# Kernel optimization log

Hardware: AMD Instinct MI355X
Metric: run time of the kernel (lower is better)

The kernel has to match this reference:

```python
import jax, jax.numpy as jnp
import numpy as np

B, S, D, H = 2, 2048, 768, 12
DH = D // H  # 64


def setup_inputs() -> dict:
    key = jax.random.key(0)
    ks = jax.random.split(key, 6)
    sd = 1.0 / np.sqrt(D)
    x = jax.random.normal(ks[0], (B, S, 3 * D), dtype=jnp.float32)
    # causal additive mask: 1.0 where attention is disallowed (future positions)
    mask = jnp.triu(jnp.ones((S, S), dtype=jnp.float32), k=1)[None, None, :, :]
    return {
        "x": x,
        "mask": mask,
        "wq": jax.random.normal(ks[1], (D, D), dtype=jnp.float32) * sd,
        "bq": jnp.zeros((D,), dtype=jnp.float32),
        "wk": jax.random.normal(ks[2], (D, D), dtype=jnp.float32) * sd,
        "bk": jnp.zeros((D,), dtype=jnp.float32),
        "wv": jax.random.normal(ks[3], (D, D), dtype=jnp.float32) * sd,
        "bv": jnp.zeros((D,), dtype=jnp.float32),
        "wc": jax.random.normal(ks[4], (D, D), dtype=jnp.float32) * sd,
        "bc": jnp.zeros((D,), dtype=jnp.float32),
    }


def _split_heads(t):
    # [B, S, D] -> [B, H, S, DH]
    return t.reshape(B, S, H, DH).transpose(0, 2, 1, 3)


def reference(x, mask, wq, bq, wk, bk, wv, bv, wc, bc):
    xq, xk, xv = jnp.split(x, 3, axis=-1)
    q = _split_heads(xq @ wq + bq)
    k = _split_heads(xk @ wk + bk)
    v = _split_heads(xv @ wv + bv)
    scores = jnp.einsum("bhqd,bhkd->bhqk", q, k) / jnp.sqrt(jnp.float32(DH))
    scores = scores + mask * (-1e9)
    attn = jax.nn.softmax(scores, axis=-1)
    out = jnp.einsum("bhqk,bhkd->bhqd", attn, v)
    out = out.transpose(0, 2, 1, 3).reshape(B, S, D)  # merge heads
    return out @ wc + bc
```

## Files before the change

### kernel.cpp

```cpp
#include <hip/hip_runtime.h>
#include <math.h>

#define S_LEN   2048
#define D_MODEL 768
#define NH      12
#define DH      64
#define BATCH   2

typedef __attribute__((ext_vector_type(4)))  float f32x4;
typedef __attribute__((ext_vector_type(16))) float f32x16;
typedef __attribute__((ext_vector_type(8)))  short bf16x8;
typedef __attribute__((ext_vector_type(4)))  short short4v;
typedef __attribute__((ext_vector_type(2)))  unsigned u32x2;

__device__ __forceinline__ short f2bf(float f) {
    union { float f; unsigned u; } v; v.f = f;
    unsigned r = (v.u + 0x7FFFu + ((v.u >> 16) & 1u)) >> 16;
    return (short)r;
}
__device__ __forceinline__ float bf2f(short s) {
    union { unsigned u; float f; } v; v.u = ((unsigned)(unsigned short)s) << 16;
    return v.f;
}
__device__ __forceinline__ unsigned cvt_pk_bf16(float lo, float hi) {
    unsigned r;
    asm("v_cvt_pk_bf16_f32 %0, %1, %2" : "=v"(r) : "v"(lo), "v"(hi));
    return r;
}
__device__ __forceinline__ void perm32swap(unsigned &a, unsigned &b) {
    asm("v_permlane32_swap_b32 %0, %1" : "+v"(a), "+v"(b));
}

#define GLOAD_LDS16(gp, lp)                                                     \
    __builtin_amdgcn_global_load_lds(                                           \
        (const __attribute__((address_space(1))) void*)(gp),                    \
        (__attribute__((address_space(3))) void*)(lp), 16, 0, 0)

__global__ __launch_bounds__(256) void convert_xw_kernel(
    const float* __restrict__ x, short* __restrict__ xb,
    const float* __restrict__ wq, const float* __restrict__ wk,
    const float* __restrict__ wv, const float* __restrict__ wc,
    short* __restrict__ wt)
{
    const int bid = blockIdx.x;
    const int t = threadIdx.x;
    if (bid < 4608) {
        const size_t i = ((size_t)bid * 256 + t) * 8;
        const f32x4 a = *(const f32x4*)(x + i);
        const f32x4 b = *(const f32x4*)(x + i + 4);
        bf16x8 r;
        r[0] = f2bf(a[0]); r[1] = f2bf(a[1]); r[2] = f2bf(a[2]); r[3] = f2bf(a[3]);
        r[4] = f2bf(b[0]); r[5] = f2bf(b[1]); r[6] = f2bf(b[2]); r[7] = f2bf(b[3]);
        *(bf16x8*)(xb + i) = r;
        return;
    }
    __shared__ float Ld[64][65];
    const int rem = bid - 4608;
    const int z  = rem / 144;
    const int yy = (rem % 144) / 12;
    const int xx = rem % 12;
    const float* W = (z == 0) ? wq : (z == 1) ? wk : (z == 2) ? wv : wc;
    short* dst = wt + (size_t)z * D_MODEL * D_MODEL;
    const int r0 = yy * 64;
    const int c0 = xx * 64;

#pragma unroll
    for (int i = 0; i < 4; ++i) {
        const int r = (t >> 4) + 16 * i;
        const int c = (t & 15) * 4;
        const float4 a = *(const float4*)(W + (size_t)(r0 + r) * D_MODEL + c0 + c);
        Ld[r][c + 0] = a.x; Ld[r][c + 1] = a.y; Ld[r][c + 2] = a.z; Ld[r][c + 3] = a.w;
    }
    __syncthreads();
#pragma unroll
    for (int i = 0; i < 4; ++i) {
        const int n = (t >> 4) + 16 * i;
        const int kq = (t & 15) * 4;
        short4v s4;
        s4[0] = f2bf(Ld[kq + 0][n]); s4[1] = f2bf(Ld[kq + 1][n]);
        s4[2] = f2bf(Ld[kq + 2][n]); s4[3] = f2bf(Ld[kq + 3][n]);
        *(short4v*)(dst + (size_t)(c0 + n) * D_MODEL + r0 + kq) = s4;
    }
}

__device__ __forceinline__ void gemm_bt_body(
    const short* __restrict__ A, int lda,
    const short* __restrict__ Bt,
    const float* __restrict__ bias,
    void* __restrict__ C, int ldc, int out_mode)
{
    __shared__ __align__(16) char ldsA[16384];
    __shared__ __align__(16) char ldsB[16384];

    const int t = threadIdx.x, lane = t & 63, w = t >> 6;
    const int l15 = lane & 15, l4 = lane >> 4;
    const int wr = w >> 1, wc = w & 1;
    const int row0 = blockIdx.y * 128, col0 = blockIdx.x * 128;

    const int srow = lane >> 3;
    const int sblk = (lane & 7) ^ srow;

    f32x4 acc[4][4];
#pragma unroll
    for (int i = 0; i < 4; ++i)
#pragma unroll
        for (int j = 0; j < 4; ++j) acc[i][j] = (f32x4){0.f, 0.f, 0.f, 0.f};

    for (int kt = 0; kt < 12; ++kt) {
        __syncthreads();
#pragma unroll
        for (int i = 0; i < 4; ++i) {
            const int row = i * 32 + w * 8 + srow;
            GLOAD_LDS16(A  + (size_t)(row0 + row) * lda + kt * 64 + sblk * 8,
                        ldsA + i * 4096 + w * 1024);
            GLOAD_LDS16(Bt + (size_t)(col0 + row) * D_MODEL + kt * 64 + sblk * 8,
                        ldsB + i * 4096 + w * 1024);
        }
        __syncthreads();

        bf16x8 af[4][2], bfr[4][2];
#pragma unroll
        for (int rb = 0; rb < 4; ++rb) {
            const int r = wr * 64 + rb * 16 + l15;
#pragma unroll
            for (int c = 0; c < 2; ++c)
                af[rb][c] = *(const bf16x8*)(ldsA + r * 128 + (((c * 4 + l4) ^ (r & 7)) << 4));
        }
#pragma unroll
        for (int cb = 0; cb < 4; ++cb) {
            const int r = wc * 64 + cb * 16 + l15;
#pragma unroll
            for (int c = 0; c < 2; ++c)
                bfr[cb][c] = *(const bf16x8*)(ldsB + r * 128 + (((c * 4 + l4) ^ (r & 7)) << 4));
        }
        __builtin_amdgcn_s_setprio(1);
#pragma unroll
        for (int rb = 0; rb < 4; ++rb)
#pragma unroll
            for (int cb = 0; cb < 4; ++cb) {
                acc[rb][cb] = __builtin_amdgcn_mfma_f32_16x16x32_bf16(
                    af[rb][0], bfr[cb][0], acc[rb][cb], 0, 0, 0);
                acc[rb][cb] = __builtin_amdgcn_mfma_f32_16x16x32_bf16(
                    af[rb][1], bfr[cb][1], acc[rb][cb], 0, 0, 0);
            }
        __builtin_amdgcn_s_setprio(0);
    }

#pragma unroll
    for (int cb = 0; cb < 4; ++cb) {
        const int col = col0 + wc * 64 + cb * 16 + l15;
        const float bv = bias[col];
        if (out_mode == 2) {
            const int h  = col >> 6, dh = col & 63;
#pragma unroll
            for (int rb = 0; rb < 4; ++rb) {
                const int row = row0 + wr * 64 + rb * 16 + 4 * l4;
                const int b   = row >> 11, s0 = row & 2047;
                short4v s4;
                s4[0] = f2bf(acc[rb][cb][0] + bv);
                s4[1] = f2bf(acc[rb][cb][1] + bv);
                s4[2] = f2bf(acc[rb][cb][2] + bv);
                s4[3] = f2bf(acc[rb][cb][3] + bv);
                *(short4v*)((short*)C + ((size_t)((b * 12 + h) * 64 + dh)) * S_LEN + s0) = s4;
            }
        } else {
#pragma unroll
            for (int rb = 0; rb < 4; ++rb)
#pragma unroll
                for (int r = 0; r < 4; ++r) {
                    const int row = row0 + wr * 64 + rb * 16 + 4 * l4 + r;
                    const float val = acc[rb][cb][r] + bv;
                    if (out_mode == 1) ((short*)C)[(size_t)row * ldc + col] = f2bf(val);
                    else               ((float*)C)[(size_t)row * ldc + col] = val;
                }
        }
    }
}

__global__ __launch_bounds__(256) void qkv_gemm_kernel(
    const short* __restrict__ xb, const short* __restrict__ wt,
    const float* __restrict__ bq, const float* __restrict__ bk,
    const float* __restrict__ bv, short* __restrict__ qkv)
{
    const int which = blockIdx.z;
    const float* bias = (which == 0) ? bq : (which == 1) ? bk : bv;
    gemm_bt_body(xb + which * D_MODEL, 3 * D_MODEL,
                 wt + (size_t)which * D_MODEL * D_MODEL, bias,
                 qkv + (size_t)which * BATCH * S_LEN * D_MODEL, D_MODEL,
                 (which == 2) ? 2 : 1);
}

__global__ __launch_bounds__(256) void proj_gemm_kernel(
    const short* __restrict__ att, const short* __restrict__ wct,
    const float* __restrict__ bc, float* __restrict__ out)
{
    gemm_bt_body(att, D_MODEL, wct, bc, out, D_MODEL, 0);
}

__global__ __launch_bounds__(512, 4) void attn_mfma_kernel(
    const short* __restrict__ q, const short* __restrict__ k,
    const short* __restrict__ vt, short* __restrict__ o)
{
    __shared__ __align__(16) char bufK[2][2][8192];
    __shared__ __align__(16) char bufV[2][2][8192];
    __shared__ float mlx[2][128];

    const int t    = threadIdx.x;
    const int lane = t & 63;
    const int w    = t >> 6;
    const int g    = w >> 2;
    const int w4   = w & 3;
    const int l31  = lane & 31;
    const int hi   = lane >> 5;
    const int r7   = l31 & 7;

    const int h  = blockIdx.y;
    const int b  = blockIdx.z;
    const int bh = h + 12 * b;
    const int qt = (bh >= 16) ? (15 - (int)blockIdx.x) : (int)blockIdx.x;
    const int nt = qt + 1;

    const size_t base   = (size_t)b * (S_LEN * D_MODEL) + h * DH;
    const size_t vtbase = (size_t)bh * DH * S_LEN;
    const int q0 = qt * 128 + w4 * 32;

    bf16x8 qf[4];
    {
        const short* qp = q + base + (size_t)(q0 + l31) * D_MODEL + 8 * hi;
#pragma unroll
        for (int dc = 0; dc < 4; ++dc) {
            bf16x8 r = *(const bf16x8*)(qp + 16 * dc);
#pragma unroll
            for (int j = 0; j < 8; ++j) r[j] = f2bf(bf2f(r[j]) * 0.125f);
            qf[dc] = r;
        }
    }

    f32x16 oT[2];
    oT[0] = (f32x16)(0.f); oT[1] = (f32x16)(0.f);
    float mrun = -1e30f, lrun = 0.f;

    const int srow = lane >> 3;
    const int sblk = (lane & 7) ^ srow;

    {
        const int tk0 = g * nt;
#pragma unroll
        for (int i = 0; i < 2; ++i) {
            const int row = i * 32 + w4 * 8 + srow;
            GLOAD_LDS16(k  + base   + (size_t)(tk0 * 64 + row) * D_MODEL + sblk * 8,
                        bufK[g][0] + i * 4096 + w4 * 1024);
            GLOAD_LDS16(vt + vtbase + (size_t)row * S_LEN + tk0 * 64 + sblk * 8,
                        bufV[g][0] + i * 4096 + w4 * 1024);
        }
        __syncthreads();
    }

    for (int i = 0; i < nt; ++i) {
        const int cur = i & 1, nxt = cur ^ 1;
        const bool have_next = (i + 1 < nt);
        const int tk = g * nt + i;

        if (have_next) {
            const int tkn = tk + 1;
#pragma unroll
            for (int j = 0; j < 2; ++j) {
                const int row = j * 32 + w4 * 8 + srow;
                GLOAD_LDS16(k  + base   + (size_t)(tkn * 64 + row) * D_MODEL + sblk * 8,
                            bufK[g][nxt] + (size_t)(j * 4096 + w4 * 1024));
                GLOAD_LDS16(vt + vtbase + (size_t)row * S_LEN + tkn * 64 + sblk * 8,
                            bufV[g][nxt] + (size_t)(j * 4096 + w4 * 1024));
            }
        }

        if (tk * 64 <= q0 + 31) {
            f32x16 cS[2];
            __builtin_amdgcn_s_setprio(1);
#pragma unroll
            for (int s = 0; s < 2; ++s) {
                f32x16 acc = (f32x16)(0.f);
#pragma unroll
                for (int dc = 0; dc < 4; ++dc) {
                    const int row = 32 * s + l31;
                    const bf16x8 kf = *(const bf16x8*)(
                        bufK[g][cur] + row * 128 + (((unsigned)(32 * dc + 16 * hi)) ^ ((unsigned)r7 << 4)));
                    acc = __builtin_amdgcn_mfma_f32_32x32x16_bf16(kf, qf[dc], acc, 0, 0, 0);
                }
                cS[s] = acc;
            }
            __builtin_amdgcn_s_setprio(0);

            if (tk * 64 + 63 > q0) {
                const int qg = q0 + l31;
#pragma unroll
                for (int s = 0; s < 2; ++s)
#pragma unroll
                    for (int rg = 0; rg < 16; ++rg) {
                        const int key = tk * 64 + 32 * s + (rg & 3) + 8 * (rg >> 2) + 4 * hi;
                        if (key > qg) cS[s][rg] = -1e30f;
                    }
            }

            float pmax = -1e30f;
#pragma unroll
            for (int s = 0; s < 2; ++s)
#pragma unroll
                for (int rg = 0; rg < 16; ++rg) pmax = fmaxf(pmax, cS[s][rg]);
            pmax = fmaxf(pmax, __shfl_xor(pmax, 32));

            if (!__all(pmax - mrun <= 8.0f)) {
                const float mnew = fmaxf(mrun, pmax);
                const float corr = __expf(mrun - mnew);
                lrun *= corr;
#pragma unroll
                for (int d0 = 0; d0 < 2; ++d0)
#pragma unroll
                    for (int rg = 0; rg < 16; ++rg) oT[d0][rg] *= corr;
                mrun = mnew;
            }
            float psum = 0.f;
#pragma unroll
            for (int s = 0; s < 2; ++s)
#pragma unroll
                for (int rg = 0; rg < 16; ++rg) {
                    const float e = __expf(cS[s][rg] - mrun);
                    cS[s][rg] = e; psum += e;
                }
            psum += __shfl_xor(psum, 32);
            lrun += psum;

            bf16x8 pfrag[4];
#pragma unroll
            for (int s = 0; s < 2; ++s)
#pragma unroll
                for (int tt = 0; tt < 2; ++tt) {
                    unsigned a0 = cvt_pk_bf16(cS[s][8 * tt + 0], cS[s][8 * tt + 1]);
                    unsigned a1 = cvt_pk_bf16(cS[s][8 * tt + 2], cS[s][8 * tt + 3]);
                    unsigned b0 = cvt_pk_bf16(cS[s][8 * tt + 4], cS[s][8 * tt + 5]);
                    unsigned b1 = cvt_pk_bf16(cS[s][8 * tt + 6], cS[s][8 * tt + 7]);
                    perm32swap(a0, b0);
                    perm32swap(a1, b1);
                    union { unsigned u[4]; bf16x8 v8; } pk;
                    pk.u[0] = a0; pk.u[1] = a1; pk.u[2] = b0; pk.u[3] = b1;
                    pfrag[2 * s + tt] = pk.v8;
                }

            __builtin_amdgcn_s_setprio(1);
#pragma unroll
            for (int d0 = 0; d0 < 2; ++d0) {
                f32x16 acc = oT[d0];
#pragma unroll
                for (int c = 0; c < 4; ++c) {
                    const int row = 32 * d0 + l31;
                    const bf16x8 vf = *(const bf16x8*)(
                        bufV[g][cur] + row * 128 + (((unsigned)(32 * c + 16 * hi)) ^ ((unsigned)r7 << 4)));
                    acc = __builtin_amdgcn_mfma_f32_32x32x16_bf16(vf, pfrag[c], acc, 0, 0, 0);
                }
                oT[d0] = acc;
            }
            __builtin_amdgcn_s_setprio(0);
        }
        __syncthreads();
    }

    if (g == 1) {
        float* ex = (float*)(&bufK[0][0][0]) + w4 * 2048;
#pragma unroll
        for (int d0 = 0; d0 < 2; ++d0)
#pragma unroll
            for (int rg = 0; rg < 16; ++rg)
                ex[(d0 * 16 + rg) * 64 + lane] = oT[d0][rg];
        if (hi == 0) {
            mlx[0][w4 * 32 + l31] = mrun;
            mlx[1][w4 * 32 + l31] = lrun;
        }
    }
    __syncthreads();

    if (g == 0) {
        const float m1  = mlx[0][w4 * 32 + l31];
        const float l1v = mlx[1][w4 * 32 + l31];
        const float M   = fmaxf(mrun, m1);
        const float a0  = __expf(mrun - M);
        const float a1  = __expf(m1 - M);
        const float inv = 1.f / (a0 * lrun + a1 * l1v);
        const float* ex = (const float*)(&bufK[0][0][0]) + w4 * 2048;

        char* wbuf = (char*)(&bufV[0][0][0]) + w4 * 4096;
#pragma unroll
        for (int d0 = 0; d0 < 2; ++d0)
#pragma unroll
            for (int gg = 0; gg < 4; ++gg) {
                float c0v = (a0 * oT[d0][4 * gg + 0] + a1 * ex[(d0 * 16 + 4 * gg + 0) * 64 + lane]) * inv;
                float c1v = (a0 * oT[d0][4 * gg + 1] + a1 * ex[(d0 * 16 + 4 * gg + 1) * 64 + lane]) * inv;
                float c2v = (a0 * oT[d0][4 * gg + 2] + a1 * ex[(d0 * 16 + 4 * gg + 2) * 64 + lane]) * inv;
                float c3v = (a0 * oT[d0][4 * gg + 3] + a1 * ex[(d0 * 16 + 4 * gg + 3) * 64 + lane]) * inv;
                u32x2 u2;
                u2[0] = cvt_pk_bf16(c0v, c1v);
                u2[1] = cvt_pk_bf16(c2v, c3v);
                const unsigned byteoff = ((unsigned)(16 * gg + 8 * hi + 64 * d0)) ^ ((unsigned)r7 << 4);
                *(u32x2*)(wbuf + l31 * 128 + byteoff) = u2;
            }
#pragma unroll
        for (int it = 0; it < 4; ++it) {
            const int R = lane >> 1;
            const unsigned lb = ((unsigned)((lane & 1) * 16 + it * 32)) ^ ((unsigned)(R & 7) << 4);
            const bf16x8 vv = *(const bf16x8*)(wbuf + R * 128 + lb);
            const int row = qt * 128 + w4 * 32 + R;
            const int col = (lane & 1) * 8 + it * 16;
            *(bf16x8*)(o + base + (size_t)row * D_MODEL + col) = vv;
        }
    }
}

extern "C" void kernel_launch(void* const* d_in, const int* in_sizes, int n_in,
                              void* d_out, int out_size, void* d_ws, size_t ws_size,
                              hipStream_t stream)
{
    const float* x  = (const float*)d_in[0];
    const float* wq = (const float*)d_in[2];
    const float* bq = (const float*)d_in[3];
    const float* wk = (const float*)d_in[4];
    const float* bk = (const float*)d_in[5];
    const float* wv = (const float*)d_in[6];
    const float* bv = (const float*)d_in[7];
    const float* wc = (const float*)d_in[8];
    const float* bc = (const float*)d_in[9];
    float* out = (float*)d_out;

    const size_t nx  = (size_t)BATCH * S_LEN * 3 * D_MODEL;
    const size_t nw  = (size_t)D_MODEL * D_MODEL;
    const size_t nqv = (size_t)BATCH * S_LEN * D_MODEL;

    short* xb  = (short*)d_ws;
    short* wt  = xb + nx;
    short* qkv = wt + 4 * nw;
    short* att = qkv + 3 * nqv;

    dim3 blk(256);
    convert_xw_kernel<<<dim3(4608 + 576), blk, 0, stream>>>(x, xb, wq, wk, wv, wc, wt);
    qkv_gemm_kernel  <<<dim3(6, 32, 3), blk, 0, stream>>>(xb, wt, bq, bk, bv, qkv);
    attn_mfma_kernel <<<dim3(16, NH, BATCH), dim3(512), 0, stream>>>(
        qkv, qkv + nqv, qkv + 2 * nqv, att);
    proj_gemm_kernel <<<dim3(6, 32), blk, 0, stream>>>(att, wt + 3 * nw, bc, out);
}
```

Baseline: 103.5 us.

## Use exp2 softmax with folded log2e scale, swizzle GEMM tiles, simplify epilogue

Folds log2(e) into the Q pre-scale so softmax can use the raw v_exp_f32 (exp2) instruction instead of __expf, and rescales the lazy-rescale threshold to match. It also remaps GEMM block indices with a stride-8 interleave, likely meant to spread neighbouring tiles across XCDs or improve L2 locality. The attention epilogue now writes 8-byte bf16 chunks straight to global memory instead of staging through LDS for 16-byte stores. The direct stores are narrower and less coalesced, and the index remap assumes the block count divides by 8.

```diff
diff --git a/kernel.cpp b/kernel.cpp
--- a/kernel.cpp
+++ b/kernel.cpp
@@ -11,7 +11,6 @@
 typedef __attribute__((ext_vector_type(16))) float f32x16;
 typedef __attribute__((ext_vector_type(8)))  short bf16x8;
 typedef __attribute__((ext_vector_type(4)))  short short4v;
-typedef __attribute__((ext_vector_type(2)))  unsigned u32x2;
 
 __device__ __forceinline__ short f2bf(float f) {
     union { float f; unsigned u; } v; v.f = f;
@@ -29,6 +28,11 @@
 }
 __device__ __forceinline__ void perm32swap(unsigned &a, unsigned &b) {
     asm("v_permlane32_swap_b32 %0, %1" : "+v"(a), "+v"(b));
+}
+__device__ __forceinline__ float exp2_fast(float x) {
+    float r;
+    asm("v_exp_f32 %0, %1" : "=v"(r) : "v"(x));
+    return r;
 }
 
 #define GLOAD_LDS16(gp, lp)                                                     \
@@ -95,7 +99,12 @@
     const int t = threadIdx.x, lane = t & 63, w = t >> 6;
     const int l15 = lane & 15, l4 = lane >> 4;
     const int wr = w >> 1, wc = w & 1;
-    const int row0 = blockIdx.y * 128, col0 = blockIdx.x * 128;
+
+    const int l  = (int)blockIdx.x + (int)gridDim.x * (int)blockIdx.y;
+    const int q8 = ((int)gridDim.x * (int)gridDim.y) >> 3;
+    const int ls = (l & 7) * q8 + (l >> 3);
+    const int row0 = (ls / (int)gridDim.x) * 128;
+    const int col0 = (ls % (int)gridDim.x) * 128;
 
     const int srow = lane >> 3;
     const int sblk = (lane & 7) ^ srow;
@@ -226,12 +235,13 @@
 
     bf16x8 qf[4];
     {
+        const float qscale = 0.18033688f;
         const short* qp = q + base + (size_t)(q0 + l31) * D_MODEL + 8 * hi;
 #pragma unroll
         for (int dc = 0; dc < 4; ++dc) {
             bf16x8 r = *(const bf16x8*)(qp + 16 * dc);
 #pragma unroll
-            for (int j = 0; j < 8; ++j) r[j] = f2bf(bf2f(r[j]) * 0.125f);
+            for (int j = 0; j < 8; ++j) r[j] = f2bf(bf2f(r[j]) * qscale);
             qf[dc] = r;
         }
     }
@@ -308,9 +318,9 @@
                 for (int rg = 0; rg < 16; ++rg) pmax = fmaxf(pmax, cS[s][rg]);
             pmax = fmaxf(pmax, __shfl_xor(pmax, 32));
 
-            if (!__all(pmax - mrun <= 8.0f)) {
+            if (!__all(pmax - mrun <= 11.52f)) {
                 const float mnew = fmaxf(mrun, pmax);
-                const float corr = __expf(mrun - mnew);
+                const float corr = exp2_fast(mrun - mnew);
                 lrun *= corr;
 #pragma unroll
                 for (int d0 = 0; d0 < 2; ++d0)
@@ -323,7 +333,7 @@
             for (int s = 0; s < 2; ++s)
 #pragma unroll
                 for (int rg = 0; rg < 16; ++rg) {
-                    const float e = __expf(cS[s][rg] - mrun);
+                    const float e = exp2_fast(cS[s][rg] - mrun);
                     cS[s][rg] = e; psum += e;
                 }
             psum += __shfl_xor(psum, 32);
@@ -378,38 +388,31 @@
     __syncthreads();
 
     if (g == 0) {
-        const float m1  = mlx[0][w4 * 32 + l31];
-        const float l1v = mlx[1][w4 * 32 + l31];
+        const int row = w4 * 32 + l31;
+        const float m1  = mlx[0][row];
+        const float l1v = mlx[1][row];
         const float M   = fmaxf(mrun, m1);
-        const float a0  = __expf(mrun - M);
-        const float a1  = __expf(m1 - M);
+        const float a0  = exp2_fast(mrun - M);
+        const float a1  = exp2_fast(m1 - M);
         const float inv = 1.f / (a0 * lrun + a1 * l1v);
+        const float c0  = a0 * inv;
+        const float c1  = a1 * inv;
         const float* ex = (const float*)(&bufK[0][0][0]) + w4 * 2048;
 
-        char* wbuf = (char*)(&bufV[0][0][0]) + w4 * 4096;
+        short* orow = o + base + (size_t)(qt * 128 + row) * D_MODEL;
 #pragma unroll
         for (int d0 = 0; d0 < 2; ++d0)
 #pragma unroll
             for (int gg = 0; gg < 4; ++gg) {
-                float c0v = (a0 * oT[d0][4 * gg + 0] + a1 * ex[(d0 * 16 + 4 * gg + 0) * 64 + lane]) * inv;
-                float c1v = (a0 * oT[d0][4 * gg + 1] + a1 * ex[(d0 * 16 + 4 * gg + 1) * 64 + lane]) * inv;
-                float c2v = (a0 * oT[d0][4 * gg + 2] + a1 * ex[(d0 * 16 + 4 * gg + 2) * 64 + lane]) * inv;
-                float c3v = (a0 * oT[d0][4 * gg + 3] + a1 * ex[(d0 * 16 + 4 * gg + 3) * 64 + lane]) * inv;
-                u32x2 u2;
-                u2[0] = cvt_pk_bf16(c0v, c1v);
-                u2[1] = cvt_pk_bf16(c2v, c3v);
-                const unsigned byteoff = ((unsigned)(16 * gg + 8 * hi + 64 * d0)) ^ ((unsigned)r7 << 4);
-                *(u32x2*)(wbuf + l31 * 128 + byteoff) = u2;
-            }
-#pragma unroll
-        for (int it = 0; it < 4; ++it) {
-            const int R = lane >> 1;
-            const unsigned lb = ((unsigned)((lane & 1) * 16 + it * 32)) ^ ((unsigned)(R & 7) << 4);
-            const bf16x8 vv = *(const bf16x8*)(wbuf + R * 128 + lb);
-            const int row = qt * 128 + w4 * 32 + R;
-            const int col = (lane & 1) * 8 + it * 16;
-            *(bf16x8*)(o + base + (size_t)row * D_MODEL + col) = vv;
-        }
+                short4v s4;
+#pragma unroll
+                for (int j = 0; j < 4; ++j) {
+                    const int rg = 4 * gg + j;
+                    const float val = c0 * oT[d0][rg] + c1 * ex[(d0 * 16 + rg) * 64 + lane];
+                    s4[j] = f2bf(val);
+                }
+                *(short4v*)(orow + 32 * d0 + 8 * gg + 4 * hi) = s4;
+            }
     }
 }
 
```

Result: faster. 97.09 us (-6.2%).
